# Performance work log

Hardware: AMD Instinct MI355X
Metric: run time of the kernel (lower is better)

## Reference

```python
import jax, jax.numpy as jnp
import numpy as np

N = 8192      # nodes
E = 262144    # edges (avg degree 32)
F_IN = 128    # input node features
H = 4         # GAT heads
C = 64        # hidden_dim
HC = H * C    # 256, GAT concat width
ED = 3        # edge_dim
NC = 8        # num_classes
NEG_SLOPE = 0.2


def setup_inputs() -> dict:
    key = jax.random.key(0)
    ks = iter(jax.random.split(key, 40))
    def w(shape, scale=0.05):
        return jax.random.normal(next(ks), shape, jnp.float32) * scale
    return {
        "x": jax.random.normal(next(ks), (N, F_IN), jnp.float32),
        "edge_attr": jax.random.uniform(next(ks), (E, ED), dtype=jnp.float32),
        # GATConv params (PyG: lin/lin_edge have no bias, final bias is [H*C])
        "gat_lin_w": w((F_IN, HC)),
        "gat_lin_edge_w": w((ED, HC)),
        "att_src": w((H, C)), "att_dst": w((H, C)), "att_edge": w((H, C)),
        "gat_bias": jnp.zeros((HC,), jnp.float32),
        "norm1_g": jnp.ones((HC,), jnp.float32), "norm1_b": jnp.zeros((HC,), jnp.float32),
        # GraphRegularizer encoder: Linear(2*HC,HC) -> ELU -> Linear(HC,1)
        "reg_w1": w((2 * HC, HC)), "reg_b1": jnp.zeros((HC,), jnp.float32),
        "reg_w2": w((HC, 1)), "reg_b2": jnp.zeros((1,), jnp.float32),
        # ConfidenceGCNConv 1: lin(HC->C), conf_lin(ED->1)
        "g1_lin_w": w((HC, C)), "g1_lin_b": jnp.zeros((C,), jnp.float32),
        "g1_conf_w": w((ED, 1)), "g1_conf_b": jnp.zeros((1,), jnp.float32),
        "norm2_g": jnp.ones((C,), jnp.float32), "norm2_b": jnp.zeros((C,), jnp.float32),
        # ConfidenceGCNConv 2: lin(C->C)
        "g2_lin_w": w((C, C)), "g2_lin_b": jnp.zeros((C,), jnp.float32),
        "g2_conf_w": w((ED, 1)), "g2_conf_b": jnp.zeros((1,), jnp.float32),
        # classifier: Linear(C,C) -> ELU -> Dropout(eval) -> Linear(C,NC)
        "cls_w1": w((C, C)), "cls_b1": jnp.zeros((C,), jnp.float32),
        "cls_w2": w((C, NC)), "cls_b2": jnp.zeros((NC,), jnp.float32),
        "edge_index": jax.random.randint(next(ks), (2, E), 0, N),
        "batch": jnp.zeros((N,), jnp.int32),
    }


def _layernorm(x, g, b, eps=1e-5):
    mu = x.mean(-1, keepdims=True)
    var = ((x - mu) ** 2).mean(-1, keepdims=True)
    return (x - mu) * jax.lax.rsqrt(var + eps) * g + b


def _gat(x, edge_index, edge_attr, lin_w, lin_edge_w, att_src, att_dst, att_edge, bias):
    """PyG GATConv (concat heads, add_self_loops=True, edge self-loop attr = mean)."""
    loop = jnp.arange(N)
    row = jnp.concatenate([edge_index[0], loop])
    col = jnp.concatenate([edge_index[1], loop])
    ea = jnp.concatenate([edge_attr, jnp.broadcast_to(edge_attr.mean(0), (N, ED))], 0)
    xs = (x @ lin_w).reshape(N, H, C)                       # [N,H,C]
    a_src = (xs * att_src).sum(-1)                          # [N,H]
    a_dst = (xs * att_dst).sum(-1)
    xe = (ea @ lin_edge_w).reshape(-1, H, C)
    a_e = (xe * att_edge).sum(-1)                           # [E+N,H]
    alpha = jax.nn.leaky_relu(a_src[row] + a_dst[col] + a_e, NEG_SLOPE)
    amax = jax.ops.segment_max(alpha, col, num_segments=N)  # softmax over edges into dst
    alpha = jnp.exp(alpha - amax[col])
    denom = jax.ops.segment_sum(alpha, col, num_segments=N)
    alpha = alpha / (denom[col] + 1e-16)
    out = jax.ops.segment_sum(xs[row] * alpha[..., None], col, num_segments=N)
    return out.reshape(N, HC) + bias


def _conf_gcn(x, row, col, edge_attr, adj_recon, lin_w, lin_b, conf_w, conf_b):
    w = jax.nn.sigmoid(edge_attr @ conf_w + conf_b)[:, 0]   # [E]
    if adj_recon is not None:
        w = (w + adj_recon[row, col]) * 0.5
    deg = jax.ops.segment_sum(jnp.ones_like(w), row, num_segments=N)
    dinv = jnp.where(deg > 0, jax.lax.rsqrt(jnp.maximum(deg, 1e-12)), 0.0)
    norm = dinv[row] * dinv[col] * w
    out = jax.ops.segment_sum(x[row] * norm[:, None], col, num_segments=N)
    return out @ lin_w + lin_b


def _regularizer(node_emb, row, col, w1, b1, w2, b2):
    pair = jnp.concatenate([node_emb[row], node_emb[col]], axis=1)  # [E,2*HC]
    h = jax.nn.elu(pair @ w1 + b1)
    prob = jax.nn.sigmoid(h @ w2 + b2)[:, 0]
    diag = jnp.arange(N)
    adj = jnp.zeros((N, N), node_emb.dtype).at[row, col].set(prob)
    return adj.at[diag, diag].set(1.0)


def reference(x, edge_attr, gat_lin_w, gat_lin_edge_w, att_src, att_dst, att_edge,
              gat_bias, norm1_g, norm1_b, reg_w1, reg_b1, reg_w2, reg_b2,
              g1_lin_w, g1_lin_b, g1_conf_w, g1_conf_b, norm2_g, norm2_b,
              g2_lin_w, g2_lin_b, g2_conf_w, g2_conf_b,
              cls_w1, cls_b1, cls_w2, cls_b2, edge_index, batch):
    row, col = edge_index[0], edge_index[1]
    h = jax.nn.elu(_gat(x, edge_index, edge_attr, gat_lin_w, gat_lin_edge_w,
                        att_src, att_dst, att_edge, gat_bias))
    h = _layernorm(h, norm1_g, norm1_b)
    adj_recon = _regularizer(h, row, col, reg_w1, reg_b1, reg_w2, reg_b2)
    h = jax.nn.elu(_conf_gcn(h, row, col, edge_attr, adj_recon,
                             g1_lin_w, g1_lin_b, g1_conf_w, g1_conf_b))
    h = _layernorm(h, norm2_g, norm2_b)
    h = _conf_gcn(h, row, col, edge_attr, adj_recon,
                  g2_lin_w, g2_lin_b, g2_conf_w, g2_conf_b)
    logits = jax.nn.elu(h @ cls_w1 + cls_b1) @ cls_w2 + cls_b2  # dropout is eval-mode no-op
    # NOTE: the Python-level BFS path reconstruction (data-dependent, returns lists
    # of ints via .item() syncs) is intentionally omitted from the tensor reference.
    return (logits, adj_recon)
```

## Files before the change

kernel.cpp:

```cpp
#include <hip/hip_runtime.h>
#include <hip/hip_fp16.h>
#include <math.h>

#define NN 8192
#define NE 262144
#define FIN 128
#define HC 256
#define CC 64
#define NCLS 8
#define NDNT 16
#define ABNT 16

constexpr size_t OFF_XS    = 0;
constexpr size_t OFF_ASRC  = OFF_XS + (size_t)NN * 256;
constexpr size_t OFF_ADST  = OFF_ASRC + (size_t)NN * 4;
constexpr size_t OFF_ALPHA = OFF_ADST + (size_t)NN * 4;
constexpr size_t OFF_CONF1 = OFF_ALPHA + (size_t)NE * 4;
constexpr size_t OFF_CONF2 = OFF_CONF1 + (size_t)NE;
constexpr size_t OFF_COEF1 = OFF_CONF2 + (size_t)NE;
constexpr size_t OFF_COEF2 = OFF_COEF1 + (size_t)NE;
constexpr size_t OFF_H1    = OFF_COEF2 + (size_t)NE;
constexpr size_t OFF_A     = OFF_H1 + (size_t)NN * 256;
constexpr size_t OFF_B     = OFF_A + (size_t)NN * 256;
constexpr size_t OFF_H2    = OFF_B + (size_t)NN * 256;
constexpr size_t OFF_DINV  = OFF_H2 + (size_t)NN * 64;
constexpr size_t OFF_SUMEA = OFF_DINV + (size_t)NN;
constexpr size_t OFF_M     = OFF_SUMEA + 4;
constexpr size_t OFF_AELOOP= OFF_M + 12;
constexpr size_t OFF_INT   = OFF_AELOOP + 4;
constexpr size_t IOFF_DEGC   = 0;
constexpr size_t IOFF_DEGR   = IOFF_DEGC + NN;
constexpr size_t IOFF_COLOFF = IOFF_DEGR + NN;
constexpr size_t IOFF_CURSOR = IOFF_COLOFF + NN + 1;
constexpr size_t IOFF_CSRROW = IOFF_CURSOR + NN;
constexpr size_t IOFF_CSREID = IOFF_CSRROW + NE;

struct alignas(8) Half4 { __half2 a, b; };
__device__ __forceinline__ float4 h4tof4(Half4 v) {
    float2 lo = __half22float2(v.a), hi = __half22float2(v.b);
    return make_float4(lo.x, lo.y, hi.x, hi.y);
}

__device__ __forceinline__ float wave_sum(float v) {
    for (int o = 32; o; o >>= 1) v += __shfl_xor(v, o);
    return v;
}
__device__ __forceinline__ float wave_max(float v) {
    for (int o = 32; o; o >>= 1) v = fmaxf(v, __shfl_xor(v, o));
    return v;
}
__device__ __forceinline__ float eluf(float v) { return v > 0.f ? v : (expf(v) - 1.f); }
__device__ __forceinline__ float sigmf(float v) { return 1.f / (1.f + expf(-v)); }

__global__ __launch_bounds__(256) void k_init(int* deg_col, int* deg_row, float* sum_ea,
                                              float* adj, const float* lew,
                                              const float* att_edge, float* M) {
    int i = blockIdx.x * blockDim.x + threadIdx.x;
    deg_col[i] = 0;
    deg_row[i] = 0;
    adj[(size_t)i * NN + i] = 1.f;
    if (i < 3) sum_ea[i] = 0.f;
    if (i < 12) {
        int d = i >> 2, h = i & 3;
        float s = 0.f;
        for (int c = 0; c < 64; c++) s = fmaf(lew[d * 256 + h * 64 + c], att_edge[h * 64 + c], s);
        M[i] = s;
    }
}

__global__ __launch_bounds__(256) void k_node(const float* __restrict__ x, const float* __restrict__ W,
                                              const float* __restrict__ att_src, const float* __restrict__ att_dst,
                                              __half* __restrict__ xs, float* __restrict__ a_src, float* __restrict__ a_dst) {
    __shared__ float xl[NDNT * FIN];
    int b = blockIdx.x, t = threadIdx.x;
    size_t base = (size_t)b * NDNT;
#pragma unroll
    for (int q = 0; q < NDNT * FIN / 256; ++q) {
        int idx = q * 256 + t;
        xl[idx] = x[base * FIN + idx];
    }
    __syncthreads();
    float acc[NDNT];
#pragma unroll
    for (int n = 0; n < NDNT; ++n) acc[n] = 0.f;
    for (int k = 0; k < FIN; ++k) {
        float wv = W[k * 256 + t];
#pragma unroll
        for (int n = 0; n < NDNT; ++n) acc[n] = fmaf(xl[n * FIN + k], wv, acc[n]);
    }
    float as = att_src[t], ad = att_dst[t];
#pragma unroll
    for (int n = 0; n < NDNT; ++n) {
        xs[(base + n) * 256 + t] = __float2half_rn(acc[n]);
        float ps = wave_sum(acc[n] * as);
        float pd = wave_sum(acc[n] * ad);
        if ((t & 63) == 0) {
            a_src[(base + n) * 4 + (t >> 6)] = ps;
            a_dst[(base + n) * 4 + (t >> 6)] = pd;
        }
    }
}

__global__ __launch_bounds__(256) void k_edge(const int* __restrict__ ei, const float* __restrict__ eattr,
                                              const float* __restrict__ M,
                                              const float* __restrict__ a_src, const float* __restrict__ a_dst,
                                              const float* __restrict__ c1w, const float* __restrict__ c1b,
                                              const float* __restrict__ c2w, const float* __restrict__ c2b,
                                              float* __restrict__ alpha, float* __restrict__ conf1, float* __restrict__ conf2,
                                              int* __restrict__ deg_col, int* __restrict__ deg_row, float* __restrict__ sum_ea) {
    int e = blockIdx.x * 256 + threadIdx.x;
    int r = ei[e], c = ei[NE + e];
    float ea0 = eattr[e * 3 + 0], ea1 = eattr[e * 3 + 1], ea2 = eattr[e * 3 + 2];
#pragma unroll
    for (int h = 0; h < 4; h++) {
        float ae = fmaf(ea0, M[0 * 4 + h], fmaf(ea1, M[1 * 4 + h], ea2 * M[2 * 4 + h]));
        float v = a_src[r * 4 + h] + a_dst[c * 4 + h] + ae;
        alpha[(size_t)e * 4 + h] = v > 0.f ? v : 0.2f * v;
    }
    conf1[e] = sigmf(fmaf(ea0, c1w[0], fmaf(ea1, c1w[1], fmaf(ea2, c1w[2], c1b[0]))));
    conf2[e] = sigmf(fmaf(ea0, c2w[0], fmaf(ea1, c2w[1], fmaf(ea2, c2w[2], c2b[0]))));
    atomicAdd(&deg_col[c], 1);
    atomicAdd(&deg_row[r], 1);
    float s0 = wave_sum(ea0), s1 = wave_sum(ea1), s2 = wave_sum(ea2);
    if ((threadIdx.x & 63) == 0) {
        atomicAdd(&sum_ea[0], s0); atomicAdd(&sum_ea[1], s1); atomicAdd(&sum_ea[2], s2);
    }
}

__global__ __launch_bounds__(256) void k_loopdinv(const float* sum_ea, const float* M, float* aeloop,
                                                  const int* deg_row, float* dinv) {
    int i = blockIdx.x * blockDim.x + threadIdx.x;
    if (i < 4) {
        float m0 = sum_ea[0] * (1.f / NE), m1 = sum_ea[1] * (1.f / NE), m2 = sum_ea[2] * (1.f / NE);
        aeloop[i] = fmaf(m0, M[0 * 4 + i], fmaf(m1, M[1 * 4 + i], m2 * M[2 * 4 + i]));
    }
    int d = deg_row[i];
    dinv[i] = d > 0 ? rsqrtf((float)d) : 0.f;
}

__global__ __launch_bounds__(256) void k_scan(const int* __restrict__ deg_col, int* __restrict__ col_off, int* __restrict__ cursor) {
    __shared__ int sd[256];
    int t = threadIdx.x;
    int base_i = t * 32;
    int loc[32];
    int s = 0;
#pragma unroll
    for (int q = 0; q < 32; q++) { loc[q] = deg_col[base_i + q]; s += loc[q]; }
    sd[t] = s;
    __syncthreads();
    for (int d = 1; d < 256; d <<= 1) {
        int v = (t >= d) ? sd[t - d] : 0;
        __syncthreads();
        sd[t] += v;
        __syncthreads();
    }
    int acc = sd[t] - s;
#pragma unroll
    for (int q = 0; q < 32; q++) { col_off[base_i + q] = acc; cursor[base_i + q] = acc; acc += loc[q]; }
    if (t == 255) col_off[NN] = acc;
}

__global__ __launch_bounds__(256) void k_fill(const int* __restrict__ ei, int* __restrict__ cursor,
                                              int* __restrict__ csr_row, int* __restrict__ csr_eid) {
    int e = blockIdx.x * 256 + threadIdx.x;
    int r = ei[e], c = ei[NE + e];
    int pos = atomicAdd(&cursor[c], 1);
    csr_row[pos] = r;
    csr_eid[pos] = e;
}

__global__ __launch_bounds__(256) void k_gat(const int* __restrict__ col_off, const int* __restrict__ csr_row,
                                             const int* __restrict__ csr_eid,
                                             const float* __restrict__ alpha, const float* __restrict__ aeloop,
                                             const float* __restrict__ a_src, const float* __restrict__ a_dst,
                                             const __half* __restrict__ xs, const float* __restrict__ gat_bias,
                                             const float* __restrict__ g, const float* __restrict__ b,
                                             __half* __restrict__ h1) {
    int i = blockIdx.x, t = threadIdx.x, h = t >> 6, lane = t & 63;
    int beg = col_off[i], end = col_off[i + 1];
    __shared__ float m_s[4], s_s[4], red[8];
    __shared__ float wl[64][5];
    float sl = a_src[i * 4 + h] + a_dst[i * 4 + h] + aeloop[h];
    sl = sl > 0.f ? sl : 0.2f * sl;
    float mx = sl;
    for (int p = beg + lane; p < end; p += 64) mx = fmaxf(mx, alpha[(size_t)csr_eid[p] * 4 + h]);
    mx = wave_max(mx);
    float ss = (lane == 0) ? expf(sl - mx) : 0.f;
    for (int p = beg + lane; p < end; p += 64) ss += expf(alpha[(size_t)csr_eid[p] * 4 + h] - mx);
    ss = wave_sum(ss);
    if (lane == 0) { m_s[h] = mx; s_s[h] = ss; }
    __syncthreads();
    float minv = m_s[h];
    float sinv = 1.f / (s_s[h] + 1e-16f);
    float acc = expf(sl - minv) * sinv * __half2float(xs[(size_t)i * 256 + t]);
    for (int cb = beg; cb < end; cb += 64) {
        int ce = min(cb + 64, end);
        int p = cb + lane;
        if (p < ce) wl[lane][h] = expf(alpha[(size_t)csr_eid[p] * 4 + h] - minv) * sinv;
        __syncthreads();
        int n = ce - cb;
        for (int q = 0; q < n; ++q)
            acc = fmaf(wl[q][h], __half2float(xs[(size_t)csr_row[cb + q] * 256 + t]), acc);
        __syncthreads();
    }
    float v = eluf(acc + gat_bias[t]);
    float s1 = wave_sum(v), s2 = wave_sum(v * v);
    if (lane == 0) { red[h] = s1; red[4 + h] = s2; }
    __syncthreads();
    float mu = (red[0] + red[1] + red[2] + red[3]) * (1.f / 256.f);
    float m2 = (red[4] + red[5] + red[6] + red[7]) * (1.f / 256.f);
    float var = m2 - mu * mu;
    float rs = rsqrtf(var + 1e-5f);
    h1[(size_t)i * 256 + t] = __float2half_rn((v - mu) * rs * g[t] + b[t]);
}

__global__ __launch_bounds__(256) void k_AB(const __half* __restrict__ h1, const float* __restrict__ w1,
                                            const float* __restrict__ b1, __half* __restrict__ A, __half* __restrict__ B) {
    __shared__ float hl[ABNT * 256];
    int bk = blockIdx.x, t = threadIdx.x;
    size_t base = (size_t)bk * ABNT;
#pragma unroll
    for (int n = 0; n < ABNT; ++n) hl[n * 256 + t] = __half2float(h1[(base + n) * 256 + t]);
    __syncthreads();
    float accA[ABNT], accB[ABNT];
    float bv = b1[t];
#pragma unroll
    for (int n = 0; n < ABNT; ++n) { accA[n] = bv; accB[n] = 0.f; }
    for (int k = 0; k < 256; ++k) {
        float wa = w1[k * 256 + t];
        float wb = w1[(256 + k) * 256 + t];
#pragma unroll
        for (int n = 0; n < ABNT; ++n) {
            float hv = hl[n * 256 + k];
            accA[n] = fmaf(hv, wa, accA[n]);
            accB[n] = fmaf(hv, wb, accB[n]);
        }
    }
#pragma unroll
    for (int n = 0; n < ABNT; ++n) {
        A[(base + n) * 256 + t] = __float2half_rn(accA[n]);
        B[(base + n) * 256 + t] = __float2half_rn(accB[n]);
    }
}

__global__ __launch_bounds__(256) void k_regc(const int* __restrict__ ei, const __half* __restrict__ A,
                                              const __half* __restrict__ B, const float* __restrict__ w2,
                                              const float* __restrict__ b2, const float* __restrict__ dinv,
                                              const float* __restrict__ conf1, const float* __restrict__ conf2,
                                              float* __restrict__ adj, float* __restrict__ coef1,
                                              float* __restrict__ coef2) {
    int t = threadIdx.x, lane = t & 63;
    int e = blockIdx.x * 4 + (t >> 6);
    int r = ei[e], c = ei[NE + e];
    float4 av = h4tof4(((const Half4*)(A + (size_t)r * 256))[lane]);
    float4 bv = h4tof4(((const Half4*)(B + (size_t)c * 256))[lane]);
    float4 w4 = ((const float4*)w2)[lane];
    float v0 = eluf(av.x + bv.x), v1 = eluf(av.y + bv.y), v2 = eluf(av.z + bv.z), v3 = eluf(av.w + bv.w);
    float s = fmaf(v0, w4.x, fmaf(v1, w4.y, fmaf(v2, w4.z, v3 * w4.w)));
    s = wave_sum(s);
    if (lane == 0) {
        float p = sigmf(s + b2[0]);
        float adjv;
        if (r != c) { adj[(size_t)r * NN + c] = p; adjv = p; }
        else adjv = 1.f;
        float base = dinv[r] * dinv[c] * 0.5f;
        coef1[e] = base * (conf1[e] + adjv);
        coef2[e] = base * (conf2[e] + adjv);
    }
}

__global__ __launch_bounds__(256) void k_gcn1(const int* __restrict__ col_off, const int* __restrict__ csr_row,
                                              const int* __restrict__ csr_eid, const float* __restrict__ coef1,
                                              const __half* __restrict__ h1, const float* __restrict__ W,
                                              const float* __restrict__ bias, const float* __restrict__ g,
                                              const float* __restrict__ bb, float* __restrict__ h2) {
    __shared__ float al[256];
    __shared__ float pl[256];
    int i = blockIdx.x, t = threadIdx.x;
    int beg = col_off[i], end = col_off[i + 1];
    float agg = 0.f;
    for (int p = beg; p < end; ++p)
        agg = fmaf(coef1[csr_eid[p]], __half2float(h1[(size_t)csr_row[p] * 256 + t]), agg);
    al[t] = agg;
    __syncthreads();
    int cc = t & 63, q = t >> 6;
    float part = 0.f;
#pragma unroll 4
    for (int k = q * 64; k < q * 64 + 64; k++) part = fmaf(al[k], W[k * 64 + cc], part);
    pl[t] = part;
    __syncthreads();
    if (t < 64) {
        float y = pl[t] + pl[t + 64] + pl[t + 128] + pl[t + 192] + bias[t];
        y = eluf(y);
        float s1 = wave_sum(y), s2 = wave_sum(y * y);
        float mu = s1 * (1.f / 64.f);
        float var = s2 * (1.f / 64.f) - mu * mu;
        h2[(size_t)i * 64 + t] = (y - mu) * rsqrtf(var + 1e-5f) * g[t] + bb[t];
    }
}

__global__ __launch_bounds__(256) void k_gcn2(const int* __restrict__ col_off, const int* __restrict__ csr_row,
                                              const int* __restrict__ csr_eid, const float* __restrict__ coef2,
                                              const float* __restrict__ h2, const float* __restrict__ g2w,
                                              const float* __restrict__ g2b, const float* __restrict__ cw1,
                                              const float* __restrict__ cb1, const float* __restrict__ cw2,
                                              const float* __restrict__ cb2, float* __restrict__ out) {
    __shared__ float zl[4][64];
    __shared__ float ul[4][64];
    __shared__ float tl[4][64];
    int t = threadIdx.x, w = t >> 6, lane = t & 63;
    int i = blockIdx.x * 4 + w;
    int beg = col_off[i], end = col_off[i + 1];
    float z = 0.f;
    for (int p = beg; p < end; ++p)
        z = fmaf(coef2[csr_eid[p]], h2[(size_t)csr_row[p] * 64 + lane], z);
    zl[w][lane] = z;
    __syncthreads();
    float u = g2b[lane];
#pragma unroll 4
    for (int k = 0; k < 64; k++) u = fmaf(zl[w][k], g2w[k * 64 + lane], u);
    ul[w][lane] = u;
    __syncthreads();
    float t1 = cb1[lane];
#pragma unroll 4
    for (int k = 0; k < 64; k++) t1 = fmaf(ul[w][k], cw1[k * 64 + lane], t1);
    t1 = eluf(t1);
    tl[w][lane] = t1;
    __syncthreads();
    if (lane < 8) {
        float o = cb2[lane];
#pragma unroll 4
        for (int k = 0; k < 64; k++) o = fmaf(tl[w][k], cw2[k * 8 + lane], o);
        out[(size_t)i * 8 + lane] = o;
    }
}

extern "C" void kernel_launch(void* const* d_in, const int* in_sizes, int n_in,
                              void* d_out, int out_size, void* d_ws, size_t ws_size,
                              hipStream_t stream) {
    const float* x           = (const float*)d_in[0];
    const float* edge_attr   = (const float*)d_in[1];
    const float* gat_lin_w   = (const float*)d_in[2];
    const float* gat_lin_edge_w = (const float*)d_in[3];
    const float* att_src     = (const float*)d_in[4];
    const float* att_dst     = (const float*)d_in[5];
    const float* att_edge    = (const float*)d_in[6];
    const float* gat_bias    = (const float*)d_in[7];
    const float* norm1_g     = (const float*)d_in[8];
    const float* norm1_b     = (const float*)d_in[9];
    const float* reg_w1      = (const float*)d_in[10];
    const float* reg_b1      = (const float*)d_in[11];
    const float* reg_w2      = (const float*)d_in[12];
    const float* reg_b2      = (const float*)d_in[13];
    const float* g1_lin_w    = (const float*)d_in[14];
    const float* g1_lin_b    = (const float*)d_in[15];
    const float* g1_conf_w   = (const float*)d_in[16];
    const float* g1_conf_b   = (const float*)d_in[17];
    const float* norm2_g     = (const float*)d_in[18];
    const float* norm2_b     = (const float*)d_in[19];
    const float* g2_lin_w    = (const float*)d_in[20];
    const float* g2_lin_b    = (const float*)d_in[21];
    const float* g2_conf_w   = (const float*)d_in[22];
    const float* g2_conf_b   = (const float*)d_in[23];
    const float* cls_w1      = (const float*)d_in[24];
    const float* cls_b1      = (const float*)d_in[25];
    const float* cls_w2      = (const float*)d_in[26];
    const float* cls_b2      = (const float*)d_in[27];
    const int*   edge_index  = (const int*)d_in[28];

    float* out = (float*)d_out;
    float* adj = out + (size_t)NN * NCLS;

    float* wsf   = (float*)d_ws;
    __half* xs   = (__half*)(wsf + OFF_XS);
    float* a_src = wsf + OFF_ASRC;
    float* a_dst = wsf + OFF_ADST;
    float* alpha = wsf + OFF_ALPHA;
    float* conf1 = wsf + OFF_CONF1;
    float* conf2 = wsf + OFF_CONF2;
    float* coef1 = wsf + OFF_COEF1;
    float* coef2 = wsf + OFF_COEF2;
    __half* h1   = (__half*)(wsf + OFF_H1);
    __half* A    = (__half*)(wsf + OFF_A);
    __half* B    = (__half*)(wsf + OFF_B);
    float* h2    = wsf + OFF_H2;
    float* dinv  = wsf + OFF_DINV;
    float* sum_ea= wsf + OFF_SUMEA;
    float* M     = wsf + OFF_M;
    float* aeloop= wsf + OFF_AELOOP;
    int* ib      = (int*)(wsf + OFF_INT);
    int* deg_col = ib + IOFF_DEGC;
    int* deg_row = ib + IOFF_DEGR;
    int* col_off = ib + IOFF_COLOFF;
    int* cursor  = ib + IOFF_CURSOR;
    int* csr_row = ib + IOFF_CSRROW;
    int* csr_eid = ib + IOFF_CSREID;

    hipMemsetAsync(adj, 0, (size_t)NN * NN * sizeof(float), stream);
    k_init<<<NN / 256, 256, 0, stream>>>(deg_col, deg_row, sum_ea, adj,
                                         gat_lin_edge_w, att_edge, M);
    k_node<<<NN / NDNT, 256, 0, stream>>>(x, gat_lin_w, att_src, att_dst, xs, a_src, a_dst);
    k_edge<<<NE / 256, 256, 0, stream>>>(edge_index, edge_attr, M, a_src, a_dst,
                                         g1_conf_w, g1_conf_b, g2_conf_w, g2_conf_b,
                                         alpha, conf1, conf2, deg_col, deg_row, sum_ea);
    k_loopdinv<<<NN / 256, 256, 0, stream>>>(sum_ea, M, aeloop, deg_row, dinv);
    k_scan<<<1, 256, 0, stream>>>(deg_col, col_off, cursor);
    k_fill<<<NE / 256, 256, 0, stream>>>(edge_index, cursor, csr_row, csr_eid);
    k_gat<<<NN, 256, 0, stream>>>(col_off, csr_row, csr_eid, alpha, aeloop, a_src, a_dst,
                                  xs, gat_bias, norm1_g, norm1_b, h1);
    k_AB<<<NN / ABNT, 256, 0, stream>>>(h1, reg_w1, reg_b1, A, B);
    k_regc<<<NE / 4, 256, 0, stream>>>(edge_index, A, B, reg_w2, reg_b2, dinv,
                                       conf1, conf2, adj, coef1, coef2);
    k_gcn1<<<NN, 256, 0, stream>>>(col_off, csr_row, csr_eid, coef1, h1,
                                   g1_lin_w, g1_lin_b, norm2_g, norm2_b, h2);
    k_gcn2<<<NN / 4, 256, 0, stream>>>(col_off, csr_row, csr_eid, coef2, h2,
                                       g2_lin_w, g2_lin_b, cls_w1, cls_b1, cls_w2, cls_b2, out);
    (void)in_sizes; (void)n_in; (void)out_size; (void)ws_size;
}
```

Measured before the change: 832.1 us.

## Split neighbor gather across waves with vectorized half4 loads in GAT and GCN1

The neighbor aggregation in the GAT and first GCN kernels is reorganized so each of the four waves handles every fourth edge and each lane loads four contiguous half features. The per-wave partial sums are then reduced through shared memory. Before, every thread walked all edges serially with scalar half loads. The aim is more memory-level parallelism and wider loads on the gather, at the cost of extra shared memory and a cross-wave reduction step.

```diff
diff --git a/kernel.cpp b/kernel.cpp
--- a/kernel.cpp
+++ b/kernel.cpp
@@ -176,10 +176,11 @@
                                              const __half* __restrict__ xs, const float* __restrict__ gat_bias,
                                              const float* __restrict__ g, const float* __restrict__ b,
                                              __half* __restrict__ h1) {
-    int i = blockIdx.x, t = threadIdx.x, h = t >> 6, lane = t & 63;
+    int i = blockIdx.x, t = threadIdx.x, h = t >> 6, lane = t & 63, w = t >> 6;
     int beg = col_off[i], end = col_off[i + 1];
     __shared__ float m_s[4], s_s[4], red[8];
     __shared__ float wl[64][5];
+    __shared__ float accL[4 * 260];
     float sl = a_src[i * 4 + h] + a_dst[i * 4 + h] + aeloop[h];
     sl = sl > 0.f ? sl : 0.2f * sl;
     float mx = sl;
@@ -192,20 +193,33 @@
     __syncthreads();
     float minv = m_s[h];
     float sinv = 1.f / (s_s[h] + 1e-16f);
-    float acc = expf(sl - minv) * sinv * __half2float(xs[(size_t)i * 256 + t]);
+    float4 acc = make_float4(0.f, 0.f, 0.f, 0.f);
+    int hh = lane >> 4;
     for (int cb = beg; cb < end; cb += 64) {
         int ce = min(cb + 64, end);
+        int n = ce - cb;
         int p = cb + lane;
         if (p < ce) wl[lane][h] = expf(alpha[(size_t)csr_eid[p] * 4 + h] - minv) * sinv;
         __syncthreads();
-        int n = ce - cb;
-        for (int q = 0; q < n; ++q)
-            acc = fmaf(wl[q][h], __half2float(xs[(size_t)csr_row[cb + q] * 256 + t]), acc);
+        for (int q = w; q < n; q += 4) {
+            int r = csr_row[cb + q];
+            float wt = wl[q][hh];
+            float4 xv = h4tof4(((const Half4*)(xs + (size_t)r * 256))[lane]);
+            acc.x = fmaf(wt, xv.x, acc.x);
+            acc.y = fmaf(wt, xv.y, acc.y);
+            acc.z = fmaf(wt, xv.z, acc.z);
+            acc.w = fmaf(wt, xv.w, acc.w);
+        }
         __syncthreads();
     }
-    float v = eluf(acc + gat_bias[t]);
+    ((float4*)(accL + w * 260))[lane] = acc;
+    __syncthreads();
+    float v = accL[t] + accL[260 + t] + accL[520 + t] + accL[780 + t];
+    float wself = expf(sl - minv) * sinv;
+    v = fmaf(wself, __half2float(xs[(size_t)i * 256 + t]), v);
+    v = eluf(v + gat_bias[t]);
     float s1 = wave_sum(v), s2 = wave_sum(v * v);
-    if (lane == 0) { red[h] = s1; red[4 + h] = s2; }
+    if (lane == 0) { red[w] = s1; red[4 + w] = s2; }
     __syncthreads();
     float mu = (red[0] + red[1] + red[2] + red[3]) * (1.f / 256.f);
     float m2 = (red[4] + red[5] + red[6] + red[7]) * (1.f / 256.f);
@@ -274,14 +288,23 @@
                                               const __half* __restrict__ h1, const float* __restrict__ W,
                                               const float* __restrict__ bias, const float* __restrict__ g,
                                               const float* __restrict__ bb, float* __restrict__ h2) {
+    __shared__ float accL[4 * 260];
     __shared__ float al[256];
     __shared__ float pl[256];
-    int i = blockIdx.x, t = threadIdx.x;
+    int i = blockIdx.x, t = threadIdx.x, w = t >> 6, lane = t & 63;
     int beg = col_off[i], end = col_off[i + 1];
-    float agg = 0.f;
-    for (int p = beg; p < end; ++p)
-        agg = fmaf(coef1[csr_eid[p]], __half2float(h1[(size_t)csr_row[p] * 256 + t]), agg);
-    al[t] = agg;
+    float4 acc = make_float4(0.f, 0.f, 0.f, 0.f);
+    for (int p = beg + w; p < end; p += 4) {
+        float cf = coef1[csr_eid[p]];
+        float4 hv = h4tof4(((const Half4*)(h1 + (size_t)csr_row[p] * 256))[lane]);
+        acc.x = fmaf(cf, hv.x, acc.x);
+        acc.y = fmaf(cf, hv.y, acc.y);
+        acc.z = fmaf(cf, hv.z, acc.z);
+        acc.w = fmaf(cf, hv.w, acc.w);
+    }
+    ((float4*)(accL + w * 260))[lane] = acc;
+    __syncthreads();
+    al[t] = accL[t] + accL[260 + t] + accL[520 + t] + accL[780 + t];
     __syncthreads();
     int cc = t & 63, q = t >> 6;
     float part = 0.f;
```

Result: no change. 824.4 us (-0.9%).
